# Kernel tuning notes

Hardware: AMD Instinct MI355X
Metric: run time of the kernel (lower is better)

Reference implementation:

```python
import jax, jax.numpy as jnp
import numpy as np

N = 50_000          # nodes
E = 1_600_000       # edges (avg degree 32)
F_IN = 8            # num_static_node_features
F_OUT = 12          # num_timesteps_in (TGCN hidden)
PERIODS = 6         # num_timesteps_out


def setup_inputs() -> dict:
    key = jax.random.key(0)
    ks = jax.random.split(key, 12)
    def n(k, shape, s=0.2):
        return jax.random.normal(k, shape, jnp.float32) * s
    return {
        "x": jax.random.normal(ks[0], (N, F_IN, PERIODS), jnp.float32),
        "edge_index": jax.random.randint(ks[1], (2, E), 0, N, dtype=jnp.int32),
        "edge_weight": jax.random.uniform(ks[2], (E,), jnp.float32),
        "att": n(ks[3], (PERIODS,), 1.0),
        "Wz": n(ks[4], (F_IN, F_OUT)), "bz": jnp.zeros((F_OUT,), jnp.float32),
        "Wr": n(ks[5], (F_IN, F_OUT)), "br": jnp.zeros((F_OUT,), jnp.float32),
        "Wh": n(ks[6], (F_IN, F_OUT)), "bh": jnp.zeros((F_OUT,), jnp.float32),
        "lzW": n(ks[7], (F_OUT, 2 * F_OUT)), "lzb": jnp.zeros((F_OUT,), jnp.float32),
        "lrW": n(ks[8], (F_OUT, 2 * F_OUT)), "lrb": jnp.zeros((F_OUT,), jnp.float32),
        "lhW": n(ks[9], (F_OUT, 2 * F_OUT)), "lhb": jnp.zeros((F_OUT,), jnp.float32),
        "linW": n(ks[10], (PERIODS, F_OUT)), "linb": jnp.zeros((PERIODS,), jnp.float32),
    }


def _gcn_norm(edge_index, edge_weight):
    # PyG gcn_norm: add self loops (weight 1.0), symmetric D^-1/2 A D^-1/2,
    # degree computed from dst (col) of edge_weight.
    src, dst = edge_index[0], edge_index[1]
    loop = jnp.arange(N, dtype=src.dtype)
    src = jnp.concatenate([src, loop])
    dst = jnp.concatenate([dst, loop])
    ew = jnp.concatenate([edge_weight, jnp.ones((N,), edge_weight.dtype)])
    deg = jax.ops.segment_sum(ew, dst, num_segments=N)
    dinv = jnp.where(deg > 0, 1.0 / jnp.sqrt(deg), 0.0)
    return src, dst, dinv[src] * ew * dinv[dst]


def _gcn_conv(xp, W, b, src, dst, norm):
    h = xp @ W                                  # [N, F_OUT]
    msg = norm[:, None] * h[src]                # gather over edges
    return jax.ops.segment_sum(msg, dst, num_segments=N) + b


def reference(x, edge_index, edge_weight, att, Wz, bz, Wr, br, Wh, bh,
              lzW, lzb, lrW, lrb, lhW, lhb, linW, linb):
    src, dst, norm = _gcn_norm(edge_index, edge_weight)
    H0 = jnp.zeros((N, F_OUT), x.dtype)  # A3TGCN passes H=None each period

    def tgcn_cell(xp):  # xp: [N, F_IN]
        Z = jax.nn.sigmoid(
            jnp.concatenate([_gcn_conv(xp, Wz, bz, src, dst, norm), H0], -1) @ lzW.T + lzb)
        R = jax.nn.sigmoid(
            jnp.concatenate([_gcn_conv(xp, Wr, br, src, dst, norm), H0], -1) @ lrW.T + lrb)
        Ht = jnp.tanh(
            jnp.concatenate([_gcn_conv(xp, Wh, bh, src, dst, norm), H0 * R], -1) @ lhW.T + lhb)
        return Z * H0 + (1.0 - Z) * Ht

    probs = jax.nn.softmax(att)                  # [P]
    Hs = jax.vmap(tgcn_cell, in_axes=2)(x)       # [P, N, F_OUT]
    H = jnp.einsum('p,pnf->nf', probs, Hs)       # attention-weighted sum
    h = jax.nn.relu(H)
    return h @ linW.T + linb                     # [N, PERIODS]
```

## Files before the change

kernel.cpp:

```cpp
#include <hip/hip_runtime.h>
#include <hip/hip_fp16.h>

#define N_NODES 50000
#define N_EDGES 1600000
#define F_IN 8
#define F_OUT 12
#define PERIODS 6
#define FP 48
#define BKT_SH 7
#define BKT_N 128
#define NBKT ((N_NODES + BKT_N - 1) / BKT_N)
#define CHK 2048
#define NCHK ((N_EDGES + CHK - 1) / CHK)
#define SEG_CAP 4736

__global__ void k_zero(unsigned int* __restrict__ cursor) {
    int i = threadIdx.x;
    if (i < NBKT) cursor[i] = 0u;
}

__global__ void __launch_bounds__(512) k_scatter(const int* __restrict__ src,
                                                 const int* __restrict__ dst,
                                                 const float* __restrict__ ew,
                                                 unsigned int* __restrict__ cursor,
                                                 unsigned long long* __restrict__ part) {
    __shared__ unsigned int h[NBKT];
    __shared__ unsigned int gbase[NBKT];
    int tid = threadIdx.x, blk = blockIdx.x;
    for (int k = tid; k < NBKT; k += 512) h[k] = 0u;
    __syncthreads();
    int base = blk * CHK;
    int bv[4]; unsigned int lr[4], lo[4], hiw[4]; bool val[4];
    #pragma unroll
    for (int u = 0; u < 4; u++) {
        int e = base + u * 512 + tid;
        val[u] = (e < N_EDGES);
        if (val[u]) {
            int s = src[e], d = dst[e];
            int b = d >> BKT_SH;
            bv[u] = b;
            lr[u] = atomicAdd(&h[b], 1u);
            lo[u] = ((unsigned int)(d & (BKT_N - 1)) << 24) | (unsigned int)s;
            hiw[u] = __float_as_uint(ew[e]);
        }
    }
    __syncthreads();
    for (int k = tid; k < NBKT; k += 512) {
        unsigned int c = h[k];
        gbase[k] = c ? atomicAdd(&cursor[k], c) : 0u;
    }
    __syncthreads();
    #pragma unroll
    for (int u = 0; u < 4; u++) {
        if (!val[u]) continue;
        unsigned int off = gbase[bv[u]] + lr[u];
        if (off < SEG_CAP)
            part[(size_t)bv[u] * SEG_CAP + off] =
                ((unsigned long long)hiw[u] << 32) | lo[u];
    }
}

__global__ void __launch_bounds__(512) k_bucket(const unsigned long long* __restrict__ part,
                                                const unsigned int* __restrict__ cursor,
                                                const float* __restrict__ x,
                                                int2* __restrict__ offs2,
                                                float* __restrict__ dinv_g,
                                                uint2* __restrict__ xs,
                                                unsigned int* __restrict__ csr4) {
    __shared__ uint2 stage[SEG_CAP];
    __shared__ unsigned int cnt[BKT_N], cnt2[BKT_N], rowstart[BKT_N], sc[BKT_N];
    __shared__ float degf[BKT_N], dinv_l[BKT_N];
    int tid = threadIdx.x, k = blockIdx.x;
    unsigned int base = (unsigned int)k * SEG_CAP;
    unsigned int m = cursor[k];
    if (m > SEG_CAP) m = SEG_CAP;
    if (tid < BKT_N) { cnt[tid] = 0u; cnt2[tid] = 0u; degf[tid] = 1.0f; }
    __syncthreads();
    for (unsigned int i = tid; i < m; i += 512) {
        unsigned long long p = part[base + i];
        unsigned int lo = (unsigned int)p;
        unsigned int hi = (unsigned int)(p >> 32);
        stage[i] = make_uint2(lo, hi);
        unsigned int j = (lo >> 24) & (BKT_N - 1);
        atomicAdd(&cnt[j], 1u);
        atomicAdd(&degf[j], __uint_as_float(hi));
    }
    __syncthreads();
    if (tid < BKT_N) sc[tid] = cnt[tid];
    __syncthreads();
    for (int off = 1; off < BKT_N; off <<= 1) {
        unsigned int u = (tid >= (unsigned)off && tid < BKT_N) ? sc[tid - off] : 0u;
        __syncthreads();
        if (tid < BKT_N) sc[tid] += u;
        __syncthreads();
    }
    if (tid < BKT_N) rowstart[tid] = sc[tid] - cnt[tid];
    __syncthreads();

    int n0 = k * BKT_N;
    int nn = N_NODES - n0; if (nn > BKT_N) nn = BKT_N;

    if (tid < BKT_N) {
        float dv = rsqrtf(degf[tid]);
        dinv_l[tid] = dv;
        if (tid < nn) {
            dinv_g[n0 + tid] = dv;
            offs2[n0 + tid] = make_int2((int)(base + rowstart[tid]),
                                        (int)(base + sc[tid]));
        }
    }

    for (unsigned int i = tid; i < m; i += 512) {
        uint2 vv = stage[i];
        unsigned int j = (vv.x >> 24) & (BKT_N - 1);
        unsigned int r = atomicAdd(&cnt2[j], 1u);
        __half hw = __float2half(__uint_as_float(vv.y));
        unsigned int entry = ((unsigned int)__half_as_ushort(hw) << 16) |
                             (vv.x & 0xFFFFu);
        csr4[base + rowstart[j] + r] = entry;
    }
    __syncthreads();

    for (int idx = tid; idx < nn * 12; idx += 512) {
        int j = idx / 12, c = idx % 12;
        int n = n0 + j;
        float di = dinv_l[j];
        const float4* xr = (const float4*)(x + (size_t)n * FP + c * 4);
        float4 a = xr[0];
        __half2 h0 = __floats2half2_rn(di * a.x, di * a.y);
        __half2 h1 = __floats2half2_rn(di * a.z, di * a.w);
        uint2 o;
        o.x = *(unsigned int*)&h0; o.y = *(unsigned int*)&h1;
        xs[(size_t)n * 12 + c] = o;
    }
}

__global__ void __launch_bounds__(256) k_gather(const uint2* __restrict__ xs,
                                                const float* __restrict__ dinv,
                                                const int2* __restrict__ offs2,
                                                const unsigned int* __restrict__ csr4,
                                                uint2* __restrict__ xagg2) {
    int t = blockIdx.x * 256 + threadIdx.x;
    if (t >= N_NODES * 12) return;
    int n = t / 12, c = t % 12;
    uint2 self = xs[(size_t)n * 12 + c];
    float2 f0 = __half22float2(*(__half2*)&self.x);
    float2 f1 = __half22float2(*(__half2*)&self.y);
    float a0 = f0.x, a1 = f0.y, a2 = f1.x, a3 = f1.y;
    int2 oe = offs2[n];
    int b = oe.x, e = oe.y;
    int kk = b;
    for (; kk + 8 <= e; kk += 8) {
        unsigned int p[8];
        uint2 v[8];
        #pragma unroll
        for (int u = 0; u < 8; u++) p[u] = csr4[kk + u];
        #pragma unroll
        for (int u = 0; u < 8; u++)
            v[u] = xs[(size_t)(p[u] & 0xFFFFu) * 12 + c];
        #pragma unroll
        for (int u = 0; u < 8; u++) {
            float w = __half2float(__ushort_as_half((unsigned short)(p[u] >> 16)));
            float2 e0 = __half22float2(*(__half2*)&v[u].x);
            float2 e1 = __half22float2(*(__half2*)&v[u].y);
            a0 += w * e0.x; a1 += w * e0.y; a2 += w * e1.x; a3 += w * e1.y;
        }
    }
    for (; kk + 4 <= e; kk += 4) {
        unsigned int p[4];
        uint2 v[4];
        #pragma unroll
        for (int u = 0; u < 4; u++) p[u] = csr4[kk + u];
        #pragma unroll
        for (int u = 0; u < 4; u++)
            v[u] = xs[(size_t)(p[u] & 0xFFFFu) * 12 + c];
        #pragma unroll
        for (int u = 0; u < 4; u++) {
            float w = __half2float(__ushort_as_half((unsigned short)(p[u] >> 16)));
            float2 e0 = __half22float2(*(__half2*)&v[u].x);
            float2 e1 = __half22float2(*(__half2*)&v[u].y);
            a0 += w * e0.x; a1 += w * e0.y; a2 += w * e1.x; a3 += w * e1.y;
        }
    }
    for (; kk < e; kk++) {
        unsigned int p = csr4[kk];
        float w = __half2float(__ushort_as_half((unsigned short)(p >> 16)));
        uint2 v = xs[(size_t)(p & 0xFFFFu) * 12 + c];
        float2 e0 = __half22float2(*(__half2*)&v.x);
        float2 e1 = __half22float2(*(__half2*)&v.y);
        a0 += w * e0.x; a1 += w * e0.y; a2 += w * e1.x; a3 += w * e1.y;
    }
    float di = dinv[n];
    __half2 o0 = __floats2half2_rn(di * a0, di * a1);
    __half2 o1 = __floats2half2_rn(di * a2, di * a3);
    uint2 o;
    o.x = *(unsigned int*)&o0; o.y = *(unsigned int*)&o1;
    xagg2[(size_t)n * 12 + c] = o;
}

__global__ void k_node(const uint2* __restrict__ xagg2, const float* __restrict__ att,
                       const float* __restrict__ Wz, const float* __restrict__ bz,
                       const float* __restrict__ Wh, const float* __restrict__ bh,
                       const float* __restrict__ lzW, const float* __restrict__ lzb,
                       const float* __restrict__ lhW, const float* __restrict__ lhb,
                       const float* __restrict__ linW, const float* __restrict__ linb,
                       float* __restrict__ out) {
    int n = blockIdx.x * blockDim.x + threadIdx.x;
    if (n >= N_NODES) return;

    float a[PERIODS];
    float m = -1e30f;
    #pragma unroll
    for (int p = 0; p < PERIODS; p++) { a[p] = att[p]; m = fmaxf(m, a[p]); }
    float se = 0.f;
    #pragma unroll
    for (int p = 0; p < PERIODS; p++) { a[p] = __expf(a[p] - m); se += a[p]; }
    float inv = 1.f / se;
    #pragma unroll
    for (int p = 0; p < PERIODS; p++) a[p] *= inv;

    float row[FP];
    const uint2* xr = xagg2 + (size_t)n * 12;
    #pragma unroll
    for (int i = 0; i < 12; i++) {
        uint2 v = xr[i];
        float2 f0 = __half22float2(*(__half2*)&v.x);
        float2 f1 = __half22float2(*(__half2*)&v.y);
        row[4 * i] = f0.x; row[4 * i + 1] = f0.y;
        row[4 * i + 2] = f1.x; row[4 * i + 3] = f1.y;
    }

    float H[F_OUT];
    #pragma unroll
    for (int j = 0; j < F_OUT; j++) H[j] = 0.f;

    for (int p = 0; p < PERIODS; p++) {
        float gz[F_OUT], gh[F_OUT];
        #pragma unroll
        for (int j = 0; j < F_OUT; j++) { gz[j] = bz[j]; gh[j] = bh[j]; }
        #pragma unroll
        for (int f = 0; f < F_IN; f++) {
            float xv = row[f * PERIODS + p];
            #pragma unroll
            for (int j = 0; j < F_OUT; j++) {
                gz[j] += xv * Wz[f * F_OUT + j];
                gh[j] += xv * Wh[f * F_OUT + j];
            }
        }
        #pragma unroll
        for (int j = 0; j < F_OUT; j++) {
            float z = lzb[j], t2 = lhb[j];
            #pragma unroll
            for (int kk = 0; kk < F_OUT; kk++) {
                z  += gz[kk] * lzW[j * (2 * F_OUT) + kk];
                t2 += gh[kk] * lhW[j * (2 * F_OUT) + kk];
            }
            float Z = 1.f / (1.f + __expf(-z));
            H[j] += a[p] * (1.f - Z) * tanhf(t2);
        }
    }

    float* op = out + (size_t)n * PERIODS;
    #pragma unroll
    for (int q = 0; q < PERIODS; q++) {
        float acc = linb[q];
        #pragma unroll
        for (int j = 0; j < F_OUT; j++)
            acc += fmaxf(H[j], 0.f) * linW[q * F_OUT + j];
        op[q] = acc;
    }
}

extern "C" void kernel_launch(void* const* d_in, const int* in_sizes, int n_in,
                              void* d_out, int out_size, void* d_ws, size_t ws_size,
                              hipStream_t stream) {
    const float* x    = (const float*)d_in[0];
    const int*   ei   = (const int*)d_in[1];
    const float* ew   = (const float*)d_in[2];
    const float* att  = (const float*)d_in[3];
    const float* Wz   = (const float*)d_in[4];
    const float* bz   = (const float*)d_in[5];
    const float* Wh   = (const float*)d_in[8];
    const float* bh   = (const float*)d_in[9];
    const float* lzW  = (const float*)d_in[10];
    const float* lzb  = (const float*)d_in[11];
    const float* lhW  = (const float*)d_in[14];
    const float* lhb  = (const float*)d_in[15];
    const float* linW = (const float*)d_in[16];
    const float* linb = (const float*)d_in[17];
    float* out = (float*)d_out;

    unsigned long long* part = (unsigned long long*)d_ws;
    unsigned int* csr4 = (unsigned int*)(part + (size_t)NBKT * SEG_CAP);
    uint2* xs = (uint2*)(csr4 + (size_t)NBKT * SEG_CAP);
    uint2* xagg2 = xs + (size_t)N_NODES * 12;
    float* dinv = (float*)(xagg2 + (size_t)N_NODES * 12);
    int2*  offs2 = (int2*)(dinv + N_NODES);
    unsigned int* cursor = (unsigned int*)(offs2 + N_NODES);

    const int* srcp = ei;
    const int* dstp = ei + N_EDGES;

    k_zero<<<1, 512, 0, stream>>>(cursor);
    k_scatter<<<NCHK, 512, 0, stream>>>(srcp, dstp, ew, cursor, part);
    k_bucket<<<NBKT, 512, 0, stream>>>(part, cursor, x, offs2, dinv, xs, csr4);
    k_gather<<<(N_NODES * 12 + 255) / 256, 256, 0, stream>>>(xs, dinv, offs2, csr4, xagg2);
    k_node<<<(N_NODES + 255) / 256, 256, 0, stream>>>(xagg2, att, Wz, bz, Wh, bh,
                                                      lzW, lzb, lhW, lhb, linW, linb, out);
}
```

Measured before the change: 214.5 us.

## Replace bucketed CSR build with per-node fixed-capacity slots via global atomics

Drops the two-pass bucket scatter and shared-memory sort. Each edge now takes a slot in a fixed 96-entry per-node row through a global atomic counter, and degree is accumulated with a global float atomic. The gather uses 16-byte loads with two lanes per row and combines them with a shuffle, and tanh is replaced by an exp-based form. The aim is fewer kernels and fewer passes over the edge list, at the cost of heavy global atomic contention, a larger padded CSR, and silently dropping edges past the cap on high-degree nodes.

```diff
diff --git a/kernel.cpp b/kernel.cpp
--- a/kernel.cpp
+++ b/kernel.cpp
@@ -7,198 +7,128 @@
 #define F_OUT 12
 #define PERIODS 6
 #define FP 48
-#define BKT_SH 7
-#define BKT_N 128
-#define NBKT ((N_NODES + BKT_N - 1) / BKT_N)
-#define CHK 2048
-#define NCHK ((N_EDGES + CHK - 1) / CHK)
-#define SEG_CAP 4736
-
-__global__ void k_zero(unsigned int* __restrict__ cursor) {
-    int i = threadIdx.x;
-    if (i < NBKT) cursor[i] = 0u;
-}
-
-__global__ void __launch_bounds__(512) k_scatter(const int* __restrict__ src,
-                                                 const int* __restrict__ dst,
-                                                 const float* __restrict__ ew,
+#define DEG_CAP 96
+
+__global__ void k_init(unsigned int* __restrict__ cursor, float* __restrict__ deg) {
+    int t = blockIdx.x * blockDim.x + threadIdx.x;
+    if (t < N_NODES) { cursor[t] = 0u; deg[t] = 1.0f; }
+}
+
+__global__ void __launch_bounds__(256) k_scatter(const int4* __restrict__ src4,
+                                                 const int4* __restrict__ dst4,
+                                                 const float4* __restrict__ ew4,
                                                  unsigned int* __restrict__ cursor,
-                                                 unsigned long long* __restrict__ part) {
-    __shared__ unsigned int h[NBKT];
-    __shared__ unsigned int gbase[NBKT];
-    int tid = threadIdx.x, blk = blockIdx.x;
-    for (int k = tid; k < NBKT; k += 512) h[k] = 0u;
-    __syncthreads();
-    int base = blk * CHK;
-    int bv[4]; unsigned int lr[4], lo[4], hiw[4]; bool val[4];
+                                                 float* __restrict__ deg,
+                                                 unsigned int* __restrict__ csr4) {
+    int t = blockIdx.x * 256 + threadIdx.x;
+    if (t >= N_EDGES / 4) return;
+    int4 ss = src4[t];
+    int4 dd = dst4[t];
+    float4 ww = ew4[t];
+    int s[4] = { ss.x, ss.y, ss.z, ss.w };
+    int d[4] = { dd.x, dd.y, dd.z, dd.w };
+    float w[4] = { ww.x, ww.y, ww.z, ww.w };
     #pragma unroll
     for (int u = 0; u < 4; u++) {
-        int e = base + u * 512 + tid;
-        val[u] = (e < N_EDGES);
-        if (val[u]) {
-            int s = src[e], d = dst[e];
-            int b = d >> BKT_SH;
-            bv[u] = b;
-            lr[u] = atomicAdd(&h[b], 1u);
-            lo[u] = ((unsigned int)(d & (BKT_N - 1)) << 24) | (unsigned int)s;
-            hiw[u] = __float_as_uint(ew[e]);
-        }
-    }
-    __syncthreads();
-    for (int k = tid; k < NBKT; k += 512) {
-        unsigned int c = h[k];
-        gbase[k] = c ? atomicAdd(&cursor[k], c) : 0u;
-    }
-    __syncthreads();
-    #pragma unroll
-    for (int u = 0; u < 4; u++) {
-        if (!val[u]) continue;
-        unsigned int off = gbase[bv[u]] + lr[u];
-        if (off < SEG_CAP)
-            part[(size_t)bv[u] * SEG_CAP + off] =
-                ((unsigned long long)hiw[u] << 32) | lo[u];
-    }
-}
-
-__global__ void __launch_bounds__(512) k_bucket(const unsigned long long* __restrict__ part,
+        unsigned int pos = atomicAdd(&cursor[d[u]], 1u);
+        atomicAdd(&deg[d[u]], w[u]);
+        if (pos < DEG_CAP) {
+            __half hw = __float2half(w[u]);
+            csr4[(size_t)d[u] * DEG_CAP + pos] =
+                ((unsigned int)__half_as_ushort(hw) << 16) | (unsigned int)s[u];
+        }
+    }
+}
+
+__global__ void __launch_bounds__(256) k_xs(const float* __restrict__ x,
+                                            const float* __restrict__ deg,
+                                            float* __restrict__ dinv,
+                                            uint4* __restrict__ xs) {
+    int t = blockIdx.x * 256 + threadIdx.x;
+    if (t >= N_NODES * 6) return;
+    int n = t / 6, c = t % 6;
+    float di = rsqrtf(deg[n]);
+    if (c == 0) dinv[n] = di;
+    const float4* xr = (const float4*)(x + (size_t)n * FP + c * 8);
+    float4 a = xr[0], b = xr[1];
+    __half2 h0 = __floats2half2_rn(di * a.x, di * a.y);
+    __half2 h1 = __floats2half2_rn(di * a.z, di * a.w);
+    __half2 h2 = __floats2half2_rn(di * b.x, di * b.y);
+    __half2 h3 = __floats2half2_rn(di * b.z, di * b.w);
+    uint4 o;
+    o.x = *(unsigned int*)&h0; o.y = *(unsigned int*)&h1;
+    o.z = *(unsigned int*)&h2; o.w = *(unsigned int*)&h3;
+    xs[t] = o;
+}
+
+__global__ void __launch_bounds__(256) k_gather(const uint4* __restrict__ xs,
+                                                const float* __restrict__ dinv,
                                                 const unsigned int* __restrict__ cursor,
-                                                const float* __restrict__ x,
-                                                int2* __restrict__ offs2,
-                                                float* __restrict__ dinv_g,
-                                                uint2* __restrict__ xs,
-                                                unsigned int* __restrict__ csr4) {
-    __shared__ uint2 stage[SEG_CAP];
-    __shared__ unsigned int cnt[BKT_N], cnt2[BKT_N], rowstart[BKT_N], sc[BKT_N];
-    __shared__ float degf[BKT_N], dinv_l[BKT_N];
-    int tid = threadIdx.x, k = blockIdx.x;
-    unsigned int base = (unsigned int)k * SEG_CAP;
-    unsigned int m = cursor[k];
-    if (m > SEG_CAP) m = SEG_CAP;
-    if (tid < BKT_N) { cnt[tid] = 0u; cnt2[tid] = 0u; degf[tid] = 1.0f; }
-    __syncthreads();
-    for (unsigned int i = tid; i < m; i += 512) {
-        unsigned long long p = part[base + i];
-        unsigned int lo = (unsigned int)p;
-        unsigned int hi = (unsigned int)(p >> 32);
-        stage[i] = make_uint2(lo, hi);
-        unsigned int j = (lo >> 24) & (BKT_N - 1);
-        atomicAdd(&cnt[j], 1u);
-        atomicAdd(&degf[j], __uint_as_float(hi));
-    }
-    __syncthreads();
-    if (tid < BKT_N) sc[tid] = cnt[tid];
-    __syncthreads();
-    for (int off = 1; off < BKT_N; off <<= 1) {
-        unsigned int u = (tid >= (unsigned)off && tid < BKT_N) ? sc[tid - off] : 0u;
-        __syncthreads();
-        if (tid < BKT_N) sc[tid] += u;
-        __syncthreads();
-    }
-    if (tid < BKT_N) rowstart[tid] = sc[tid] - cnt[tid];
-    __syncthreads();
-
-    int n0 = k * BKT_N;
-    int nn = N_NODES - n0; if (nn > BKT_N) nn = BKT_N;
-
-    if (tid < BKT_N) {
-        float dv = rsqrtf(degf[tid]);
-        dinv_l[tid] = dv;
-        if (tid < nn) {
-            dinv_g[n0 + tid] = dv;
-            offs2[n0 + tid] = make_int2((int)(base + rowstart[tid]),
-                                        (int)(base + sc[tid]));
-        }
-    }
-
-    for (unsigned int i = tid; i < m; i += 512) {
-        uint2 vv = stage[i];
-        unsigned int j = (vv.x >> 24) & (BKT_N - 1);
-        unsigned int r = atomicAdd(&cnt2[j], 1u);
-        __half hw = __float2half(__uint_as_float(vv.y));
-        unsigned int entry = ((unsigned int)__half_as_ushort(hw) << 16) |
-                             (vv.x & 0xFFFFu);
-        csr4[base + rowstart[j] + r] = entry;
-    }
-    __syncthreads();
-
-    for (int idx = tid; idx < nn * 12; idx += 512) {
-        int j = idx / 12, c = idx % 12;
-        int n = n0 + j;
-        float di = dinv_l[j];
-        const float4* xr = (const float4*)(x + (size_t)n * FP + c * 4);
-        float4 a = xr[0];
-        __half2 h0 = __floats2half2_rn(di * a.x, di * a.y);
-        __half2 h1 = __floats2half2_rn(di * a.z, di * a.w);
-        uint2 o;
-        o.x = *(unsigned int*)&h0; o.y = *(unsigned int*)&h1;
-        xs[(size_t)n * 12 + c] = o;
-    }
-}
-
-__global__ void __launch_bounds__(256) k_gather(const uint2* __restrict__ xs,
-                                                const float* __restrict__ dinv,
-                                                const int2* __restrict__ offs2,
                                                 const unsigned int* __restrict__ csr4,
-                                                uint2* __restrict__ xagg2) {
+                                                uint4* __restrict__ xagg) {
     int t = blockIdx.x * 256 + threadIdx.x;
     if (t >= N_NODES * 12) return;
-    int n = t / 12, c = t % 12;
-    uint2 self = xs[(size_t)n * 12 + c];
-    float2 f0 = __half22float2(*(__half2*)&self.x);
-    float2 f1 = __half22float2(*(__half2*)&self.y);
-    float a0 = f0.x, a1 = f0.y, a2 = f1.x, a3 = f1.y;
-    int2 oe = offs2[n];
-    int b = oe.x, e = oe.y;
-    int kk = b;
-    for (; kk + 8 <= e; kk += 8) {
-        unsigned int p[8];
-        uint2 v[8];
-        #pragma unroll
-        for (int u = 0; u < 8; u++) p[u] = csr4[kk + u];
-        #pragma unroll
-        for (int u = 0; u < 8; u++)
-            v[u] = xs[(size_t)(p[u] & 0xFFFFu) * 12 + c];
-        #pragma unroll
-        for (int u = 0; u < 8; u++) {
-            float w = __half2float(__ushort_as_half((unsigned short)(p[u] >> 16)));
-            float2 e0 = __half22float2(*(__half2*)&v[u].x);
-            float2 e1 = __half22float2(*(__half2*)&v[u].y);
-            a0 += w * e0.x; a1 += w * e0.y; a2 += w * e1.x; a3 += w * e1.y;
-        }
-    }
-    for (; kk + 4 <= e; kk += 4) {
-        unsigned int p[4];
-        uint2 v[4];
-        #pragma unroll
-        for (int u = 0; u < 4; u++) p[u] = csr4[kk + u];
+    int n = t / 12, r = t % 12, c = r >> 1, g = r & 1;
+    unsigned int cnt = cursor[n];
+    if (cnt > DEG_CAP) cnt = DEG_CAP;
+    const unsigned int* row = csr4 + (size_t)n * DEG_CAP;
+    float a0 = 0.f, a1 = 0.f, a2 = 0.f, a3 = 0.f;
+    float a4 = 0.f, a5 = 0.f, a6 = 0.f, a7 = 0.f;
+    int kk = 0;
+    for (; kk + 8 <= (int)cnt; kk += 8) {
+        unsigned int p[4]; uint4 v[4];
+        #pragma unroll
+        for (int u = 0; u < 4; u++) p[u] = row[kk + 2 * u + g];
         #pragma unroll
         for (int u = 0; u < 4; u++)
-            v[u] = xs[(size_t)(p[u] & 0xFFFFu) * 12 + c];
+            v[u] = xs[(size_t)(p[u] & 0xFFFFu) * 6 + c];
         #pragma unroll
         for (int u = 0; u < 4; u++) {
             float w = __half2float(__ushort_as_half((unsigned short)(p[u] >> 16)));
             float2 e0 = __half22float2(*(__half2*)&v[u].x);
             float2 e1 = __half22float2(*(__half2*)&v[u].y);
+            float2 e2 = __half22float2(*(__half2*)&v[u].z);
+            float2 e3 = __half22float2(*(__half2*)&v[u].w);
             a0 += w * e0.x; a1 += w * e0.y; a2 += w * e1.x; a3 += w * e1.y;
-        }
-    }
-    for (; kk < e; kk++) {
-        unsigned int p = csr4[kk];
+            a4 += w * e2.x; a5 += w * e2.y; a6 += w * e3.x; a7 += w * e3.y;
+        }
+    }
+    for (int j = kk + g; j < (int)cnt; j += 2) {
+        unsigned int p = row[j];
         float w = __half2float(__ushort_as_half((unsigned short)(p >> 16)));
-        uint2 v = xs[(size_t)(p & 0xFFFFu) * 12 + c];
+        uint4 v = xs[(size_t)(p & 0xFFFFu) * 6 + c];
         float2 e0 = __half22float2(*(__half2*)&v.x);
         float2 e1 = __half22float2(*(__half2*)&v.y);
+        float2 e2 = __half22float2(*(__half2*)&v.z);
+        float2 e3 = __half22float2(*(__half2*)&v.w);
         a0 += w * e0.x; a1 += w * e0.y; a2 += w * e1.x; a3 += w * e1.y;
-    }
-    float di = dinv[n];
-    __half2 o0 = __floats2half2_rn(di * a0, di * a1);
-    __half2 o1 = __floats2half2_rn(di * a2, di * a3);
-    uint2 o;
-    o.x = *(unsigned int*)&o0; o.y = *(unsigned int*)&o1;
-    xagg2[(size_t)n * 12 + c] = o;
-}
-
-__global__ void k_node(const uint2* __restrict__ xagg2, const float* __restrict__ att,
+        a4 += w * e2.x; a5 += w * e2.y; a6 += w * e3.x; a7 += w * e3.y;
+    }
+    a0 += __shfl_xor(a0, 1); a1 += __shfl_xor(a1, 1);
+    a2 += __shfl_xor(a2, 1); a3 += __shfl_xor(a3, 1);
+    a4 += __shfl_xor(a4, 1); a5 += __shfl_xor(a5, 1);
+    a6 += __shfl_xor(a6, 1); a7 += __shfl_xor(a7, 1);
+    if (g == 0) {
+        uint4 sf = xs[(size_t)n * 6 + c];
+        float2 s0 = __half22float2(*(__half2*)&sf.x);
+        float2 s1 = __half22float2(*(__half2*)&sf.y);
+        float2 s2 = __half22float2(*(__half2*)&sf.z);
+        float2 s3 = __half22float2(*(__half2*)&sf.w);
+        a0 += s0.x; a1 += s0.y; a2 += s1.x; a3 += s1.y;
+        a4 += s2.x; a5 += s2.y; a6 += s3.x; a7 += s3.y;
+        float di = dinv[n];
+        __half2 h0 = __floats2half2_rn(di * a0, di * a1);
+        __half2 h1 = __floats2half2_rn(di * a2, di * a3);
+        __half2 h2 = __floats2half2_rn(di * a4, di * a5);
+        __half2 h3 = __floats2half2_rn(di * a6, di * a7);
+        uint4 o;
+        o.x = *(unsigned int*)&h0; o.y = *(unsigned int*)&h1;
+        o.z = *(unsigned int*)&h2; o.w = *(unsigned int*)&h3;
+        xagg[(size_t)n * 6 + c] = o;
+    }
+}
+
+__global__ void k_node(const uint4* __restrict__ xagg, const float* __restrict__ att,
                        const float* __restrict__ Wz, const float* __restrict__ bz,
                        const float* __restrict__ Wh, const float* __restrict__ bh,
                        const float* __restrict__ lzW, const float* __restrict__ lzb,
@@ -220,14 +150,18 @@
     for (int p = 0; p < PERIODS; p++) a[p] *= inv;
 
     float row[FP];
-    const uint2* xr = xagg2 + (size_t)n * 12;
-    #pragma unroll
-    for (int i = 0; i < 12; i++) {
-        uint2 v = xr[i];
+    const uint4* xr = xagg + (size_t)n * 6;
+    #pragma unroll
+    for (int i = 0; i < 6; i++) {
+        uint4 v = xr[i];
         float2 f0 = __half22float2(*(__half2*)&v.x);
         float2 f1 = __half22float2(*(__half2*)&v.y);
-        row[4 * i] = f0.x; row[4 * i + 1] = f0.y;
-        row[4 * i + 2] = f1.x; row[4 * i + 3] = f1.y;
+        float2 f2 = __half22float2(*(__half2*)&v.z);
+        float2 f3 = __half22float2(*(__half2*)&v.w);
+        row[8 * i + 0] = f0.x; row[8 * i + 1] = f0.y;
+        row[8 * i + 2] = f1.x; row[8 * i + 3] = f1.y;
+        row[8 * i + 4] = f2.x; row[8 * i + 5] = f2.y;
+        row[8 * i + 6] = f3.x; row[8 * i + 7] = f3.y;
     }
 
     float H[F_OUT];
@@ -256,7 +190,9 @@
                 t2 += gh[kk] * lhW[j * (2 * F_OUT) + kk];
             }
             float Z = 1.f / (1.f + __expf(-z));
-            H[j] += a[p] * (1.f - Z) * tanhf(t2);
+            float e2 = __expf(2.f * t2);
+            float th = 1.f - __fdividef(2.f, e2 + 1.f);
+            H[j] += a[p] * (1.f - Z) * th;
         }
     }
 
@@ -290,21 +226,21 @@
     const float* linb = (const float*)d_in[17];
     float* out = (float*)d_out;
 
-    unsigned long long* part = (unsigned long long*)d_ws;
-    unsigned int* csr4 = (unsigned int*)(part + (size_t)NBKT * SEG_CAP);
-    uint2* xs = (uint2*)(csr4 + (size_t)NBKT * SEG_CAP);
-    uint2* xagg2 = xs + (size_t)N_NODES * 12;
-    float* dinv = (float*)(xagg2 + (size_t)N_NODES * 12);
-    int2*  offs2 = (int2*)(dinv + N_NODES);
-    unsigned int* cursor = (unsigned int*)(offs2 + N_NODES);
+    uint4* xs   = (uint4*)d_ws;
+    uint4* xagg = xs + (size_t)N_NODES * 6;
+    unsigned int* csr4 = (unsigned int*)(xagg + (size_t)N_NODES * 6);
+    unsigned int* cursor = csr4 + (size_t)N_NODES * DEG_CAP;
+    float* deg  = (float*)(cursor + N_NODES);
+    float* dinv = deg + N_NODES;
 
     const int* srcp = ei;
     const int* dstp = ei + N_EDGES;
 
-    k_zero<<<1, 512, 0, stream>>>(cursor);
-    k_scatter<<<NCHK, 512, 0, stream>>>(srcp, dstp, ew, cursor, part);
-    k_bucket<<<NBKT, 512, 0, stream>>>(part, cursor, x, offs2, dinv, xs, csr4);
-    k_gather<<<(N_NODES * 12 + 255) / 256, 256, 0, stream>>>(xs, dinv, offs2, csr4, xagg2);
-    k_node<<<(N_NODES + 255) / 256, 256, 0, stream>>>(xagg2, att, Wz, bz, Wh, bh,
+    k_init<<<(N_NODES + 511) / 512, 512, 0, stream>>>(cursor, deg);
+    k_scatter<<<(N_EDGES / 4 + 255) / 256, 256, 0, stream>>>(
+        (const int4*)srcp, (const int4*)dstp, (const float4*)ew, cursor, deg, csr4);
+    k_xs<<<(N_NODES * 6 + 255) / 256, 256, 0, stream>>>(x, deg, dinv, xs);
+    k_gather<<<(N_NODES * 12 + 255) / 256, 256, 0, stream>>>(xs, dinv, cursor, csr4, xagg);
+    k_node<<<(N_NODES + 255) / 256, 256, 0, stream>>>(xagg, att, Wz, bz, Wh, bh,
                                                       lzW, lzb, lhW, lhb, linW, linb, out);
 }
```

After: 323.9 us. 51.0% more time.
